# Kernel tuning notes

Hardware: AMD Instinct MI355X
Metric: run time of the kernel (lower is better)

Reference implementation:

```python
import jax, jax.numpy as jnp
import numpy as np
import math

B, S, DIM, HEADS, HEAD_DIM = 2, 2048, 1024, 16, 64
ROT_DIM, ROPE_THETA = 64, 10000.0


def make_rope(seq_len):
    # DitRotary.forward: theta over half rotary_dim, duplicated interleaved pairs
    theta = 1.0 / (ROPE_THETA ** (np.arange(0, ROT_DIM, 2, dtype=np.float32) / ROT_DIM))
    pos = np.arange(seq_len, dtype=np.float32).reshape(-1, 1)
    idx = pos * theta  # [S, 32]
    cos = np.stack((np.cos(idx), np.cos(idx)), axis=-1).reshape(seq_len, -1)  # [S, 64]
    sin = np.stack((np.sin(idx), np.sin(idx)), axis=-1).reshape(seq_len, -1)
    # unsqueeze(2).unsqueeze(1) -> [1, S, 1, 64]
    return jnp.asarray(cos)[None, :, None, :], jnp.asarray(sin)[None, :, None, :]


def rotate_half(x):
    # interleaved-pair rotation: (x1, x2) -> (-x2, x1)
    x = x.reshape(*x.shape[:-1], -1, 2)
    x1, x2 = x[..., 0], x[..., 1]
    return jnp.stack((-x2, x1), axis=-1).reshape(*x.shape[:-2], -1)


def apply_rotary(x, cos, sin):
    return x * cos + rotate_half(x) * sin


def setup_inputs() -> dict:
    key = jax.random.key(0)
    ks = jax.random.split(key, 8)
    sc = 1.0 / math.sqrt(DIM)
    x = jax.random.normal(ks[0], (B, S, DIM), dtype=jnp.float32)
    cos, sin = make_rope(S)
    Wq = jax.random.normal(ks[1], (DIM, DIM), dtype=jnp.float32) * sc
    bq = jnp.zeros((DIM,), jnp.float32)
    Wk = jax.random.normal(ks[2], (DIM, DIM), dtype=jnp.float32) * sc
    bk = jnp.zeros((DIM,), jnp.float32)
    Wv = jax.random.normal(ks[3], (DIM, DIM), dtype=jnp.float32) * sc
    bv = jnp.zeros((DIM,), jnp.float32)
    Wo = jax.random.normal(ks[4], (DIM, DIM), dtype=jnp.float32) * sc
    bo = jnp.zeros((DIM,), jnp.float32)
    mask = jnp.ones((B, 1, 1, S), dtype=bool)
    return {"x": x, "cos": cos, "sin": sin, "Wq": Wq, "bq": bq, "Wk": Wk,
            "bk": bk, "Wv": Wv, "bv": bv, "Wo": Wo, "bo": bo, "mask": mask}


def reference(x, cos, sin, Wq, bq, Wk, bk, Wv, bv, Wo, bo, mask):
    b, s, _ = x.shape
    q = (x @ Wq.T + bq).reshape(b, s, HEADS, HEAD_DIM)
    k = (x @ Wk.T + bk).reshape(b, s, HEADS, HEAD_DIM)
    v = (x @ Wv.T + bv).reshape(b, s, HEADS, HEAD_DIM)
    # partial rotary: applied only to head index 0 (dim 2 of [B,S,H,D])
    q = jnp.concatenate([apply_rotary(q[:, :, :1, :], cos, sin), q[:, :, 1:, :]], axis=2)
    k = jnp.concatenate([apply_rotary(k[:, :, :1, :], cos, sin), k[:, :, 1:, :]], axis=2)
    # [B,H,S,D]
    q = q.transpose(0, 2, 1, 3)
    k = k.transpose(0, 2, 1, 3)
    v = v.transpose(0, 2, 1, 3)
    neg = jnp.finfo(jnp.float32).min
    attn_mask = jnp.where(mask, 0.0, neg)  # ~mask * finfo.min
    scores = jnp.einsum("bhsd,bhtd->bhst", q, k) / math.sqrt(HEAD_DIM)
    scores = scores + attn_mask
    probs = jax.nn.softmax(scores.astype(jnp.float32), axis=-1).astype(q.dtype)
    out = jnp.einsum("bhst,bhtd->bhsd", probs, v)
    out = out.transpose(0, 2, 1, 3).reshape(b, s, HEADS * HEAD_DIM)
    return out @ Wo.T + bo
```

## Files before the change

### kernel.cpp

```cpp
#include <hip/hip_runtime.h>
#include <hip/hip_bf16.h>


typedef __attribute__((ext_vector_type(8))) __bf16 bf16x8;
typedef __attribute__((ext_vector_type(4))) __bf16 bf16x4;
typedef __attribute__((ext_vector_type(4))) float f32x4;
typedef __attribute__((ext_vector_type(4))) short s16x4;

#define NB_B 2
#define NB_S 2048
#define NB_DIM 1024
#define NB_H 16
#define NB_HD 64
#define NB_BS (NB_B * NB_S)

__device__ __forceinline__ void async_cp16(const __bf16* g, __bf16* l) {
    __builtin_amdgcn_global_load_lds(
        (const __attribute__((address_space(1))) unsigned int*)g,
        (__attribute__((address_space(3))) unsigned int*)l, 16, 0, 0);
}

__global__ __launch_bounds__(256) void cvt_kernel(
    const float* __restrict__ x,  const float* __restrict__ wq,
    const float* __restrict__ wk, const float* __restrict__ wv,
    const float* __restrict__ wo,
    __bf16* __restrict__ xb,  __bf16* __restrict__ wqb,
    __bf16* __restrict__ wkb, __bf16* __restrict__ wvb,
    __bf16* __restrict__ wob) {
    const int XQ = (NB_BS * NB_DIM) / 4;
    const int WQ = (NB_DIM * NB_DIM) / 4;
    int i = blockIdx.x * 256 + threadIdx.x;
    const float* src; __bf16* dst; int off;
    if (i < XQ)              { src = x;  dst = xb;  off = i; }
    else if (i < XQ + WQ)    { src = wq; dst = wqb; off = i - XQ; }
    else if (i < XQ + 2*WQ)  { src = wk; dst = wkb; off = i - XQ - WQ; }
    else if (i < XQ + 3*WQ)  { src = wv; dst = wvb; off = i - XQ - 2*WQ; }
    else                     { src = wo; dst = wob; off = i - XQ - 3*WQ; }
    f32x4 v = *(const f32x4*)(src + (size_t)off * 4);
    bf16x4 b;
#pragma unroll
    for (int j = 0; j < 4; ++j) b[j] = (__bf16)v[j];
    *(bf16x4*)(dst + (size_t)off * 4) = b;
}

__global__ __launch_bounds__(256) void gemm_qkv_kernel(
    const __bf16* __restrict__ A,
    const float* __restrict__ cosb, const float* __restrict__ sinb,
    const __bf16* __restrict__ Wq, const float* __restrict__ bq, __bf16* __restrict__ qbuf,
    const __bf16* __restrict__ Wk, const float* __restrict__ bk, __bf16* __restrict__ kbuf,
    const __bf16* __restrict__ Wv, const float* __restrict__ bv, __bf16* __restrict__ vtbuf) {
    constexpr int K = 1024;
    __shared__ __align__(16) __bf16 As[128][64];
    __shared__ __align__(16) __bf16 Bs[128][64];

    const int z = blockIdx.z;
    const __bf16* W; const float* bias;
    if (z == 0)      { W = Wq; bias = bq; }
    else if (z == 1) { W = Wk; bias = bk; }
    else             { W = Wv; bias = bv; }

    const int tid = threadIdx.x;
    const int lane = tid & 63;
    const int w = tid >> 6;
    const int wm = w >> 1, wn = w & 1;
    const int row16 = lane & 15, quad = lane >> 4;
    const int r7 = row16 & 7;
    const int m0 = blockIdx.x * 128, n0 = blockIdx.y * 128;

    f32x4 acc[4][4] = {};

    for (int kt = 0; kt < K; kt += 64) {
        __syncthreads();
#pragma unroll
        for (int i = 0; i < 4; ++i) {
            int c = tid + i * 256;
            int row = c >> 3, g = c & 7;
            int gcol = (g ^ (row & 7)) << 3;
            async_cp16(A + (size_t)(m0 + row) * K + kt + gcol, &As[row][g << 3]);
            async_cp16(W + (size_t)(n0 + row) * K + kt + gcol, &Bs[row][g << 3]);
        }
        __syncthreads();

        bf16x8 af[4][2], bfr[4][2];
#pragma unroll
        for (int t = 0; t < 4; ++t)
#pragma unroll
            for (int kk = 0; kk < 2; ++kk) {
                af[t][kk]  = *(const bf16x8*)&As[wm * 64 + t * 16 + row16][((kk * 4 + quad) ^ r7) << 3];
                bfr[t][kk] = *(const bf16x8*)&Bs[wn * 64 + t * 16 + row16][((kk * 4 + quad) ^ r7) << 3];
            }
        __builtin_amdgcn_s_setprio(1);
#pragma unroll
        for (int mt = 0; mt < 4; ++mt)
#pragma unroll
            for (int nt = 0; nt < 4; ++nt)
#pragma unroll
                for (int kk = 0; kk < 2; ++kk)
                    acc[mt][nt] = __builtin_amdgcn_mfma_f32_16x16x32_bf16(af[mt][kk], bfr[nt][kk], acc[mt][nt], 0, 0, 0);
        __builtin_amdgcn_s_setprio(0);
    }

    if (z == 2) {
#pragma unroll
        for (int mt = 0; mt < 4; ++mt) {
            int row = m0 + wm * 64 + mt * 16 + quad * 4;
            int b = row >> 11, s = row & (NB_S - 1);
#pragma unroll
            for (int nt = 0; nt < 4; ++nt) {
                int col = n0 + wn * 64 + nt * 16 + row16;
                float bv = bias[col];
                bf16x4 pack;
#pragma unroll
                for (int r = 0; r < 4; ++r) pack[r] = (__bf16)(acc[mt][nt][r] + bv);
                *(bf16x4*)&vtbuf[(size_t)b * (NB_DIM * NB_S) + (size_t)col * NB_S + s] = pack;
            }
        }
    } else {
        __bf16* C = (z == 0) ? qbuf : kbuf;
        const bool rope = (n0 == 0) && (wn == 0);
#pragma unroll
        for (int mt = 0; mt < 4; ++mt) {
            int row = m0 + wm * 64 + mt * 16 + quad * 4;
#pragma unroll
            for (int nt = 0; nt < 4; ++nt) {
                int col = n0 + wn * 64 + nt * 16 + row16;
                float bv = bias[col];
#pragma unroll
                for (int r = 0; r < 4; ++r) {
                    float val = acc[mt][nt][r] + bv;
                    if (rope) {
                        float part = __shfl_xor(val, 1, 64);
                        int srow = (row + r) & (NB_S - 1);
                        float c  = cosb[srow * 64 + col];
                        float sn = sinb[srow * 64 + col];
                        val = (lane & 1) ? (val * c + part * sn) : (val * c - part * sn);
                    }
                    C[(size_t)(row + r) * NB_DIM + col] = (__bf16)val;
                }
            }
        }
    }
}

__global__ __launch_bounds__(256) void gemm_o_kernel(
    const __bf16* __restrict__ A, const __bf16* __restrict__ W,
    const float* __restrict__ bias, float* __restrict__ C) {
    constexpr int K = 1024;
    __shared__ __align__(16) __bf16 As[128][64];
    __shared__ __align__(16) __bf16 Bs[64][64];

    const int tid = threadIdx.x;
    const int lane = tid & 63;
    const int w = tid >> 6;
    const int row16 = lane & 15, quad = lane >> 4;
    const int r7 = row16 & 7;
    const int m0 = blockIdx.x * 128, n0 = blockIdx.y * 64;

    f32x4 acc[2][4] = {};

    for (int kt = 0; kt < K; kt += 64) {
        __syncthreads();
#pragma unroll
        for (int i = 0; i < 4; ++i) {
            int c = tid + i * 256;
            int row = c >> 3, g = c & 7;
            int gcol = (g ^ (row & 7)) << 3;
            async_cp16(A + (size_t)(m0 + row) * K + kt + gcol, &As[row][g << 3]);
        }
#pragma unroll
        for (int i = 0; i < 2; ++i) {
            int c = tid + i * 256;
            int row = c >> 3, g = c & 7;
            int gcol = (g ^ (row & 7)) << 3;
            async_cp16(W + (size_t)(n0 + row) * K + kt + gcol, &Bs[row][g << 3]);
        }
        __syncthreads();

        bf16x8 af[2][2], bfr[4][2];
#pragma unroll
        for (int t = 0; t < 2; ++t)
#pragma unroll
            for (int kk = 0; kk < 2; ++kk)
                af[t][kk] = *(const bf16x8*)&As[w * 32 + t * 16 + row16][((kk * 4 + quad) ^ r7) << 3];
#pragma unroll
        for (int nt = 0; nt < 4; ++nt)
#pragma unroll
            for (int kk = 0; kk < 2; ++kk)
                bfr[nt][kk] = *(const bf16x8*)&Bs[nt * 16 + row16][((kk * 4 + quad) ^ r7) << 3];
        __builtin_amdgcn_s_setprio(1);
#pragma unroll
        for (int mt = 0; mt < 2; ++mt)
#pragma unroll
            for (int nt = 0; nt < 4; ++nt)
#pragma unroll
                for (int kk = 0; kk < 2; ++kk)
                    acc[mt][nt] = __builtin_amdgcn_mfma_f32_16x16x32_bf16(af[mt][kk], bfr[nt][kk], acc[mt][nt], 0, 0, 0);
        __builtin_amdgcn_s_setprio(0);
    }

#pragma unroll
    for (int mt = 0; mt < 2; ++mt) {
        int row = m0 + w * 32 + mt * 16 + quad * 4;
#pragma unroll
        for (int nt = 0; nt < 4; ++nt) {
            int col = n0 + nt * 16 + row16;
            float bv = bias[col];
#pragma unroll
            for (int r = 0; r < 4; ++r)
                C[(size_t)(row + r) * NB_DIM + col] = acc[mt][nt][r] + bv;
        }
    }
}

__global__ __launch_bounds__(512) void attn_kernel(const __bf16* __restrict__ qb,
                                                   const __bf16* __restrict__ kb,
                                                   const __bf16* __restrict__ vtb,
                                                   __bf16* __restrict__ ob) {
    __shared__ __align__(16) __bf16 Ks[2][128][72];
    __shared__ __align__(16) __bf16 Vts[2][64][132];

    const int tid = threadIdx.x;
    const int lane = tid & 63;
    const int w = tid >> 6;
    const int row16 = lane & 15, quad = lane >> 4;
    const int bh = blockIdx.x;
    const int b = bh >> 4, h = bh & 15;
    const int q0 = blockIdx.y * 256 + w * 32;

    const size_t headoff = (size_t)b * NB_S * NB_DIM + (size_t)h * NB_HD;
    const size_t vtoff = (size_t)b * (NB_DIM * NB_S) + (size_t)(h * NB_HD) * NB_S;

    const float qscale = 0.18033688011112042f;
    bf16x8 qf[2][2];
#pragma unroll
    for (int m = 0; m < 2; ++m)
#pragma unroll
        for (int hh = 0; hh < 2; ++hh) {
            bf16x8 v = *(const bf16x8*)(qb + headoff + (size_t)(q0 + m * 16 + row16) * NB_DIM + hh * 32 + quad * 8);
#pragma unroll
            for (int j = 0; j < 8; ++j) v[j] = (__bf16)((float)v[j] * qscale);
            qf[m][hh] = v;
        }

    f32x4 o[2][4] = {};
    f32x4 ol[2] = {};

    const __bf16 oneb = __builtin_bit_cast(__bf16, (short)0x3F80);
    bf16x8 ones8;
#pragma unroll
    for (int j = 0; j < 8; ++j) ones8[j] = oneb;

    bf16x8 kreg[2], vreg[2];
#pragma unroll
    for (int i = 0; i < 2; ++i) {
        int c = tid + i * 512;
        kreg[i] = *(const bf16x8*)(kb + headoff + (size_t)(c >> 3) * NB_DIM + ((c & 7) << 3));
        vreg[i] = *(const bf16x8*)(vtb + vtoff + (size_t)(c >> 4) * NB_S + ((c & 15) << 3));
    }
#pragma unroll
    for (int i = 0; i < 2; ++i) {
        int c = tid + i * 512;
        *(bf16x8*)&Ks[0][c >> 3][(c & 7) << 3] = kreg[i];
        bf16x4 lo, hi;
#pragma unroll
        for (int j = 0; j < 4; ++j) { lo[j] = vreg[i][j]; hi[j] = vreg[i][j + 4]; }
        *(bf16x4*)&Vts[0][c >> 4][(c & 15) << 3] = lo;
        *(bf16x4*)&Vts[0][c >> 4][((c & 15) << 3) + 4] = hi;
    }
#pragma unroll
    for (int i = 0; i < 2; ++i) {
        int c = tid + i * 512;
        kreg[i] = *(const bf16x8*)(kb + headoff + (size_t)(128 + (c >> 3)) * NB_DIM + ((c & 7) << 3));
        vreg[i] = *(const bf16x8*)(vtb + vtoff + (size_t)(c >> 4) * NB_S + 128 + ((c & 15) << 3));
    }
    asm volatile("s_waitcnt lgkmcnt(0)" ::: "memory");
    __builtin_amdgcn_s_barrier();

    for (int kt = 0; kt < 16; ++kt) {
        const int cur = kt & 1;
        if (kt < 15) {
#pragma unroll
            for (int i = 0; i < 2; ++i) {
                int c = tid + i * 512;
                *(bf16x8*)&Ks[cur ^ 1][c >> 3][(c & 7) << 3] = kreg[i];
                bf16x4 lo, hi;
#pragma unroll
                for (int j = 0; j < 4; ++j) { lo[j] = vreg[i][j]; hi[j] = vreg[i][j + 4]; }
                *(bf16x4*)&Vts[cur ^ 1][c >> 4][(c & 15) << 3] = lo;
                *(bf16x4*)&Vts[cur ^ 1][c >> 4][((c & 15) << 3) + 4] = hi;
            }
        }
        if (kt < 14) {
            int base = (kt + 2) * 128;
#pragma unroll
            for (int i = 0; i < 2; ++i) {
                int c = tid + i * 512;
                kreg[i] = *(const bf16x8*)(kb + headoff + (size_t)(base + (c >> 3)) * NB_DIM + ((c & 7) << 3));
                vreg[i] = *(const bf16x8*)(vtb + vtoff + (size_t)(c >> 4) * NB_S + base + ((c & 15) << 3));
            }
        }

        bf16x8 pf8[2][4];
#pragma unroll
        for (int t = 0; t < 8; ++t) {
            f32x4 s0 = {}, s1 = {};
            __builtin_amdgcn_s_setprio(1);
#pragma unroll
            for (int hh = 0; hh < 2; ++hh) {
                bf16x8 kf = *(const bf16x8*)&Ks[cur][t * 16 + row16][hh * 32 + quad * 8];
                s0 = __builtin_amdgcn_mfma_f32_16x16x32_bf16(kf, qf[0][hh], s0, 0, 0, 0);
                s1 = __builtin_amdgcn_mfma_f32_16x16x32_bf16(kf, qf[1][hh], s1, 0, 0, 0);
            }
            __builtin_amdgcn_s_setprio(0);
#pragma unroll
            for (int r = 0; r < 4; ++r) {
                pf8[0][t >> 1][(t & 1) * 4 + r] = (__bf16)__builtin_amdgcn_exp2f(s0[r]);
                pf8[1][t >> 1][(t & 1) * 4 + r] = (__bf16)__builtin_amdgcn_exp2f(s1[r]);
            }
        }

        __builtin_amdgcn_s_setprio(1);
#pragma unroll
        for (int tp = 0; tp < 4; ++tp) {
            ol[0] = __builtin_amdgcn_mfma_f32_16x16x32_bf16(pf8[0][tp], ones8, ol[0], 0, 0, 0);
            ol[1] = __builtin_amdgcn_mfma_f32_16x16x32_bf16(pf8[1][tp], ones8, ol[1], 0, 0, 0);
        }
#pragma unroll
        for (int nt = 0; nt < 4; ++nt)
#pragma unroll
            for (int tp = 0; tp < 4; ++tp) {
                bf16x4 vlo = *(const bf16x4*)&Vts[cur][nt * 16 + row16][tp * 32 + quad * 4];
                bf16x4 vhi = *(const bf16x4*)&Vts[cur][nt * 16 + row16][tp * 32 + 16 + quad * 4];
                bf16x8 vfp;
#pragma unroll
                for (int j = 0; j < 4; ++j) { vfp[j] = vlo[j]; vfp[4 + j] = vhi[j]; }
                o[0][nt] = __builtin_amdgcn_mfma_f32_16x16x32_bf16(pf8[0][tp], vfp, o[0][nt], 0, 0, 0);
                o[1][nt] = __builtin_amdgcn_mfma_f32_16x16x32_bf16(pf8[1][tp], vfp, o[1][nt], 0, 0, 0);
            }
        __builtin_amdgcn_s_setprio(0);

        if (kt < 15) {
            asm volatile("s_waitcnt lgkmcnt(0)" ::: "memory");
            __builtin_amdgcn_s_barrier();
        }
    }

#pragma unroll
    for (int m = 0; m < 2; ++m)
#pragma unroll
        for (int r = 0; r < 4; ++r) {
            float inv = 1.f / ol[m][r];
            int row = q0 + m * 16 + quad * 4 + r;
#pragma unroll
            for (int nt = 0; nt < 4; ++nt)
                ob[headoff + (size_t)row * NB_DIM + nt * 16 + row16] = (__bf16)(o[m][nt][r] * inv);
        }
}

extern "C" void kernel_launch(void* const* d_in, const int* in_sizes, int n_in,
                              void* d_out, int out_size, void* d_ws, size_t ws_size,
                              hipStream_t stream) {
    const float* x    = (const float*)d_in[0];
    const float* cosb = (const float*)d_in[1];
    const float* sinb = (const float*)d_in[2];
    const float* Wq   = (const float*)d_in[3];
    const float* bq   = (const float*)d_in[4];
    const float* Wk   = (const float*)d_in[5];
    const float* bk   = (const float*)d_in[6];
    const float* Wv   = (const float*)d_in[7];
    const float* bv   = (const float*)d_in[8];
    const float* Wo   = (const float*)d_in[9];
    const float* bo   = (const float*)d_in[10];

    __bf16* qbuf  = (__bf16*)d_ws;
    __bf16* kbuf  = qbuf + (size_t)NB_BS * NB_DIM;
    __bf16* vtbuf = kbuf + (size_t)NB_BS * NB_DIM;
    __bf16* abuf  = vtbuf + (size_t)NB_BS * NB_DIM;
    __bf16* xb    = abuf + (size_t)NB_BS * NB_DIM;
    __bf16* wqb   = xb + (size_t)NB_BS * NB_DIM;
    __bf16* wkb   = wqb + (size_t)NB_DIM * NB_DIM;
    __bf16* wvb   = wkb + (size_t)NB_DIM * NB_DIM;
    __bf16* wob   = wvb + (size_t)NB_DIM * NB_DIM;

    const int XQ = (NB_BS * NB_DIM) / 4, WQ = (NB_DIM * NB_DIM) / 4;
    cvt_kernel<<<(XQ + 4 * WQ) / 256, 256, 0, stream>>>(x, Wq, Wk, Wv, Wo,
                                                        xb, wqb, wkb, wvb, wob);

    dim3 gqkv(NB_BS / 128, NB_DIM / 128, 3);
    gemm_qkv_kernel<<<gqkv, 256, 0, stream>>>(xb, cosb, sinb,
                                              wqb, bq, qbuf,
                                              wkb, bk, kbuf,
                                              wvb, bv, vtbuf);

    attn_kernel<<<dim3(NB_B * NB_H, NB_S / 256), 512, 0, stream>>>(qbuf, kbuf, vtbuf, abuf);

    dim3 go(NB_BS / 128, NB_DIM / 64);
    gemm_o_kernel<<<go, 256, 0, stream>>>(abuf, wob, bo, (float*)d_out);
}
```

Baseline: 192.5 us.

## Fuse fp32-to-bf16 conversion into GEMM tile loads, drop cvt kernel

Removes the separate conversion kernel that cast x and all four weight matrices to bf16. The QKV and output-projection GEMMs now read fp32 directly into registers, convert to bf16, and write into the swizzled LDS tiles. The next tile is prefetched into registers while the current one is computed. This saves a launch and a full write-plus-read of the bf16 copies. In exchange, the GEMMs read twice as many bytes per tile, repeat the cast work in every block that reloads a tile, use more registers, and replace the async global-to-LDS copies with register staging.

```diff
diff --git a/kernel.cpp b/kernel.cpp
--- a/kernel.cpp
+++ b/kernel.cpp
@@ -20,41 +20,18 @@
         (__attribute__((address_space(3))) unsigned int*)l, 16, 0, 0);
 }
 
-__global__ __launch_bounds__(256) void cvt_kernel(
-    const float* __restrict__ x,  const float* __restrict__ wq,
-    const float* __restrict__ wk, const float* __restrict__ wv,
-    const float* __restrict__ wo,
-    __bf16* __restrict__ xb,  __bf16* __restrict__ wqb,
-    __bf16* __restrict__ wkb, __bf16* __restrict__ wvb,
-    __bf16* __restrict__ wob) {
-    const int XQ = (NB_BS * NB_DIM) / 4;
-    const int WQ = (NB_DIM * NB_DIM) / 4;
-    int i = blockIdx.x * 256 + threadIdx.x;
-    const float* src; __bf16* dst; int off;
-    if (i < XQ)              { src = x;  dst = xb;  off = i; }
-    else if (i < XQ + WQ)    { src = wq; dst = wqb; off = i - XQ; }
-    else if (i < XQ + 2*WQ)  { src = wk; dst = wkb; off = i - XQ - WQ; }
-    else if (i < XQ + 3*WQ)  { src = wv; dst = wvb; off = i - XQ - 2*WQ; }
-    else                     { src = wo; dst = wob; off = i - XQ - 3*WQ; }
-    f32x4 v = *(const f32x4*)(src + (size_t)off * 4);
-    bf16x4 b;
-#pragma unroll
-    for (int j = 0; j < 4; ++j) b[j] = (__bf16)v[j];
-    *(bf16x4*)(dst + (size_t)off * 4) = b;
-}
-
 __global__ __launch_bounds__(256) void gemm_qkv_kernel(
-    const __bf16* __restrict__ A,
+    const float* __restrict__ A,
     const float* __restrict__ cosb, const float* __restrict__ sinb,
-    const __bf16* __restrict__ Wq, const float* __restrict__ bq, __bf16* __restrict__ qbuf,
-    const __bf16* __restrict__ Wk, const float* __restrict__ bk, __bf16* __restrict__ kbuf,
-    const __bf16* __restrict__ Wv, const float* __restrict__ bv, __bf16* __restrict__ vtbuf) {
+    const float* __restrict__ Wq, const float* __restrict__ bq, __bf16* __restrict__ qbuf,
+    const float* __restrict__ Wk, const float* __restrict__ bk, __bf16* __restrict__ kbuf,
+    const float* __restrict__ Wv, const float* __restrict__ bv, __bf16* __restrict__ vtbuf) {
     constexpr int K = 1024;
     __shared__ __align__(16) __bf16 As[128][64];
     __shared__ __align__(16) __bf16 Bs[128][64];
 
     const int z = blockIdx.z;
-    const __bf16* W; const float* bias;
+    const float* W; const float* bias;
     if (z == 0)      { W = Wq; bias = bq; }
     else if (z == 1) { W = Wk; bias = bk; }
     else             { W = Wv; bias = bv; }
@@ -68,18 +45,38 @@
     const int m0 = blockIdx.x * 128, n0 = blockIdx.y * 128;
 
     f32x4 acc[4][4] = {};
-
+    f32x4 areg[8], breg[8];
+
+    auto load_tiles = [&](int kt) {
+#pragma unroll
+        for (int i = 0; i < 8; ++i) {
+            int s = tid + i * 256;
+            int row = s >> 4, f4 = s & 15;
+            areg[i] = *(const f32x4*)(A + (size_t)(m0 + row) * K + kt + f4 * 4);
+            breg[i] = *(const f32x4*)(W + (size_t)(n0 + row) * K + kt + f4 * 4);
+        }
+    };
+    auto write_tiles = [&]() {
+#pragma unroll
+        for (int i = 0; i < 8; ++i) {
+            int s = tid + i * 256;
+            int row = s >> 4, f4 = s & 15;
+            int g = f4 >> 1, sub = f4 & 1;
+            int co = ((g ^ (row & 7)) << 3) + sub * 4;
+            bf16x4 av, bv;
+#pragma unroll
+            for (int j = 0; j < 4; ++j) { av[j] = (__bf16)areg[i][j]; bv[j] = (__bf16)breg[i][j]; }
+            *(bf16x4*)&As[row][co] = av;
+            *(bf16x4*)&Bs[row][co] = bv;
+        }
+    };
+
+    load_tiles(0);
     for (int kt = 0; kt < K; kt += 64) {
         __syncthreads();
-#pragma unroll
-        for (int i = 0; i < 4; ++i) {
-            int c = tid + i * 256;
-            int row = c >> 3, g = c & 7;
-            int gcol = (g ^ (row & 7)) << 3;
-            async_cp16(A + (size_t)(m0 + row) * K + kt + gcol, &As[row][g << 3]);
-            async_cp16(W + (size_t)(n0 + row) * K + kt + gcol, &Bs[row][g << 3]);
-        }
+        write_tiles();
         __syncthreads();
+        if (kt + 64 < K) load_tiles(kt + 64);
 
         bf16x8 af[4][2], bfr[4][2];
 #pragma unroll
@@ -143,7 +140,7 @@
 }
 
 __global__ __launch_bounds__(256) void gemm_o_kernel(
-    const __bf16* __restrict__ A, const __bf16* __restrict__ W,
+    const __bf16* __restrict__ A, const float* __restrict__ W,
     const float* __restrict__ bias, float* __restrict__ C) {
     constexpr int K = 1024;
     __shared__ __align__(16) __bf16 As[128][64];
@@ -157,7 +154,18 @@
     const int m0 = blockIdx.x * 128, n0 = blockIdx.y * 64;
 
     f32x4 acc[2][4] = {};
-
+    f32x4 breg[4];
+
+    auto load_b = [&](int kt) {
+#pragma unroll
+        for (int i = 0; i < 4; ++i) {
+            int s = tid + i * 256;
+            int row = s >> 4, f4 = s & 15;
+            breg[i] = *(const f32x4*)(W + (size_t)(n0 + row) * K + kt + f4 * 4);
+        }
+    };
+
+    load_b(0);
     for (int kt = 0; kt < K; kt += 64) {
         __syncthreads();
 #pragma unroll
@@ -168,13 +176,18 @@
             async_cp16(A + (size_t)(m0 + row) * K + kt + gcol, &As[row][g << 3]);
         }
 #pragma unroll
-        for (int i = 0; i < 2; ++i) {
-            int c = tid + i * 256;
-            int row = c >> 3, g = c & 7;
-            int gcol = (g ^ (row & 7)) << 3;
-            async_cp16(W + (size_t)(n0 + row) * K + kt + gcol, &Bs[row][g << 3]);
+        for (int i = 0; i < 4; ++i) {
+            int s = tid + i * 256;
+            int row = s >> 4, f4 = s & 15;
+            int g = f4 >> 1, sub = f4 & 1;
+            int co = ((g ^ (row & 7)) << 3) + sub * 4;
+            bf16x4 bv;
+#pragma unroll
+            for (int j = 0; j < 4; ++j) bv[j] = (__bf16)breg[i][j];
+            *(bf16x4*)&Bs[row][co] = bv;
         }
         __syncthreads();
+        if (kt + 64 < K) load_b(kt + 64);
 
         bf16x8 af[2][2], bfr[4][2];
 #pragma unroll
@@ -376,24 +389,15 @@
     __bf16* kbuf  = qbuf + (size_t)NB_BS * NB_DIM;
     __bf16* vtbuf = kbuf + (size_t)NB_BS * NB_DIM;
     __bf16* abuf  = vtbuf + (size_t)NB_BS * NB_DIM;
-    __bf16* xb    = abuf + (size_t)NB_BS * NB_DIM;
-    __bf16* wqb   = xb + (size_t)NB_BS * NB_DIM;
-    __bf16* wkb   = wqb + (size_t)NB_DIM * NB_DIM;
-    __bf16* wvb   = wkb + (size_t)NB_DIM * NB_DIM;
-    __bf16* wob   = wvb + (size_t)NB_DIM * NB_DIM;
-
-    const int XQ = (NB_BS * NB_DIM) / 4, WQ = (NB_DIM * NB_DIM) / 4;
-    cvt_kernel<<<(XQ + 4 * WQ) / 256, 256, 0, stream>>>(x, Wq, Wk, Wv, Wo,
-                                                        xb, wqb, wkb, wvb, wob);
 
     dim3 gqkv(NB_BS / 128, NB_DIM / 128, 3);
-    gemm_qkv_kernel<<<gqkv, 256, 0, stream>>>(xb, cosb, sinb,
-                                              wqb, bq, qbuf,
-                                              wkb, bk, kbuf,
-                                              wvb, bv, vtbuf);
+    gemm_qkv_kernel<<<gqkv, 256, 0, stream>>>(x, cosb, sinb,
+                                              Wq, bq, qbuf,
+                                              Wk, bk, kbuf,
+                                              Wv, bv, vtbuf);
 
     attn_kernel<<<dim3(NB_B * NB_H, NB_S / 256), 512, 0, stream>>>(qbuf, kbuf, vtbuf, abuf);
 
     dim3 go(NB_BS / 128, NB_DIM / 64);
-    gemm_o_kernel<<<go, 256, 0, stream>>>(abuf, wob, bo, (float*)d_out);
+    gemm_o_kernel<<<go, 256, 0, stream>>>(abuf, Wo, bo, (float*)d_out);
 }
```

Result: slower. 220.0 us (+14.3%).
